# Optimization experiments

Measured on AMD Instinct MI355X. Metric: run time of the kernel, lower is better.

Reference implementation:

```python
import jax, jax.numpy as jnp
import numpy as np

PAD_VAL = -10000.0


def setup_inputs() -> dict:
    key = jax.random.key(0)
    k1, k2 = jax.random.split(key)
    B, C, H, W = 16, 3, 256, 256
    predicted = jax.random.normal(k1, (B, C, H, W), dtype=jnp.float32)
    ground_truth = jax.random.normal(k2, (B, C, H, W), dtype=jnp.float32)
    return {"predicted": predicted, "ground_truth": ground_truth, "nh": 5, "nw": 5}


def reference(predicted, ground_truth, nh, nw):
    # Faithful to torch: ConstantPad2d((v_pad, v_pad, h_pad, h_pad)) pads
    # W by v_pad = nh//2 and H by h_pad = nw//2 (symmetric when nh == nw).
    v_pad = nh // 2
    h_pad = nw // 2
    B, C, H, W = ground_truth.shape
    gt_pad = jnp.pad(
        ground_truth,
        ((0, 0), (0, 0), (h_pad, h_pad), (v_pad, v_pad)),
        constant_values=PAD_VAL,
    )
    # nh*nw shifted views of the padded ground truth: [B, C, H, W, nh*nw]
    refs = jnp.stack(
        [gt_pad[:, :, i:i + H, j:j + W] for i in range(nh) for j in range(nw)],
        axis=-1,
    )
    # L1 distance over channels for each neighbor shift: [B, H, W, nh*nw]
    norms = jnp.sum(jnp.abs(refs - predicted[..., None]), axis=1)
    # min over neighborhood, then mean over batch/spatial
    return jnp.mean(jnp.min(norms, axis=-1))
```

## Files before the change

kernel.cpp:

```cpp
#include <hip/hip_runtime.h>
#include <math.h>

#define PAD_VAL (-10000.0f)

constexpr int Cc = 3, Hh = 256, Ww = 256, Bb = 16;
constexpr int TW = 64;
constexpr int TH = 16;
constexpr int PXT = 4;
constexpr int LDSH = TH + 4;
constexpr int LDSW = 76;
constexpr int F4_PER_ROW = 18;
constexpr int NSLOT = Cc * LDSH * F4_PER_ROW;


__global__ __launch_bounds__(256) void nnloss_main(
    const float* __restrict__ pred, const float* __restrict__ gt,
    float* __restrict__ partial)
{
    __shared__ float sh[Cc][LDSH][LDSW];
    __shared__ float wsum[4];

    const int bx = blockIdx.x, by = blockIdx.y, b = blockIdx.z;
    const int cbase = bx * TW, rbase = by * TH;
    const int tid = threadIdx.x;
    const size_t base = (size_t)b * Cc * Hh * Ww;

    const bool interior = (bx >= 1) & (bx <= 2) & (by >= 1) & (by <= 14);
    if (interior) {
#pragma unroll
        for (int it = 0; it < 5; ++it) {
            int s = tid + it * 256;
            if (s < NSLOT) {
                int ch  = s / (LDSH * F4_PER_ROW);
                int rem = s - ch * (LDSH * F4_PER_ROW);
                int lr  = rem / F4_PER_ROW;
                int lc4 = rem - lr * F4_PER_ROW;
                int r   = rbase + lr - 2;
                int c   = cbase + lc4 * 4 - 4;
                float4 v = *reinterpret_cast<const float4*>(
                    &gt[base + ((size_t)ch * Hh + r) * Ww + c]);
                *reinterpret_cast<float4*>(&sh[ch][lr][lc4 * 4]) = v;
            }
        }
    } else {
#pragma unroll
        for (int it = 0; it < 5; ++it) {
            int s = tid + it * 256;
            if (s < NSLOT) {
                int ch  = s / (LDSH * F4_PER_ROW);
                int rem = s - ch * (LDSH * F4_PER_ROW);
                int lr  = rem / F4_PER_ROW;
                int lc4 = rem - lr * F4_PER_ROW;
                int r   = rbase + lr - 2;
                int c0  = cbase + lc4 * 4 - 4;
                float4 v;
                float* vp = reinterpret_cast<float*>(&v);
                const bool rok = (unsigned)r < (unsigned)Hh;
#pragma unroll
                for (int k = 0; k < 4; ++k) {
                    int c = c0 + k;
                    vp[k] = (rok && (unsigned)c < (unsigned)Ww)
                          ? gt[base + ((size_t)ch * Hh + r) * Ww + c] : PAD_VAL;
                }
                *reinterpret_cast<float4*>(&sh[ch][lr][lc4 * 4]) = v;
            }
        }
    }
    __syncthreads();

    const int gx  = tid & 15;
    const int gy  = tid >> 4;
    const int w0  = cbase + gx * PXT;
    const int row = rbase + gy;

    float p[Cc][PXT];
#pragma unroll
    for (int ch = 0; ch < Cc; ++ch) {
        float4 a = *reinterpret_cast<const float4*>(
            &pred[base + ((size_t)ch * Hh + row) * Ww + w0]);
        p[ch][0] = a.x; p[ch][1] = a.y; p[ch][2] = a.z; p[ch][3] = a.w;
    }

    float best[PXT];
#pragma unroll
    for (int px = 0; px < PXT; ++px) best[px] = 3.0e38f;

#pragma unroll
    for (int di = 0; di < 5; ++di) {
        float wv[Cc][12];
#pragma unroll
        for (int ch = 0; ch < Cc; ++ch) {
            const float4* q = reinterpret_cast<const float4*>(&sh[ch][gy + di][4 * gx]);
            float4 q0 = q[0], q1 = q[1], q2 = q[2];
            wv[ch][0] = q0.x; wv[ch][1]  = q0.y; wv[ch][2]  = q0.z; wv[ch][3]  = q0.w;
            wv[ch][4] = q1.x; wv[ch][5]  = q1.y; wv[ch][6]  = q1.z; wv[ch][7]  = q1.w;
            wv[ch][8] = q2.x; wv[ch][9]  = q2.y; wv[ch][10] = q2.z; wv[ch][11] = q2.w;
        }
#pragma unroll
        for (int dj = 0; dj < 5; ++dj) {
#pragma unroll
            for (int px = 0; px < PXT; ++px) {
                float s = fabsf(wv[0][px + dj + 2] - p[0][px])
                        + fabsf(wv[1][px + dj + 2] - p[1][px])
                        + fabsf(wv[2][px + dj + 2] - p[2][px]);
                best[px] = fminf(best[px], s);
            }
        }
    }

    float t = (best[0] + best[1]) + (best[2] + best[3]);
#pragma unroll
    for (int off = 32; off; off >>= 1) t += __shfl_down(t, off, 64);
    if ((tid & 63) == 0) wsum[tid >> 6] = t;
    __syncthreads();
    if (tid == 0) {
        int pid = (blockIdx.z * gridDim.y + blockIdx.y) * gridDim.x + blockIdx.x;
        partial[pid] = (wsum[0] + wsum[1]) + (wsum[2] + wsum[3]);
    }
}

__global__ __launch_bounds__(256) void nnloss_reduce(
    const float* __restrict__ partial, int n, float* __restrict__ out)
{
    __shared__ float ws[4];
    float t = 0.0f;
    for (int i = threadIdx.x; i < n; i += 256) t += partial[i];
#pragma unroll
    for (int off = 32; off; off >>= 1) t += __shfl_down(t, off, 64);
    if ((threadIdx.x & 63) == 0) ws[threadIdx.x >> 6] = t;
    __syncthreads();
    if (threadIdx.x == 0)
        out[0] = ((ws[0] + ws[1]) + (ws[2] + ws[3]))
               * (1.0f / ((float)Bb * (float)Hh * (float)Ww));
}

extern "C" void kernel_launch(void* const* d_in, const int* in_sizes, int n_in,
                              void* d_out, int out_size, void* d_ws, size_t ws_size,
                              hipStream_t stream) {
    const float* pred = (const float*)d_in[0];
    const float* gt   = (const float*)d_in[1];
    float* out     = (float*)d_out;
    float* partial = (float*)d_ws;

    dim3 grid(Ww / TW, Hh / TH, Bb);
    nnloss_main<<<grid, 256, 0, stream>>>(pred, gt, partial);
    nnloss_reduce<<<1, 256, 0, stream>>>(partial, 1024, out);
}
```

Measured before the change: 17.35 us.

## Compute two output rows per thread to reuse LDS window loads across rows

Halves the block to 128 threads, each handling a 2x4 pixel patch instead of 1x4, so each LDS window row is loaded once and reused by both output rows (6 row loads instead of 10). The separate interior and border gt-loading paths are merged into one float4 load guarded per vector, and the pred loads are issued before the LDS fill. This cuts LDS traffic and load count per pixel but raises register use and halves the threads per block, which may lower occupancy and latency hiding.

```diff
diff --git a/kernel.cpp b/kernel.cpp
--- a/kernel.cpp
+++ b/kernel.cpp
@@ -6,116 +6,104 @@
 constexpr int Cc = 3, Hh = 256, Ww = 256, Bb = 16;
 constexpr int TW = 64;
 constexpr int TH = 16;
-constexpr int PXT = 4;
 constexpr int LDSH = TH + 4;
 constexpr int LDSW = 76;
 constexpr int F4_PER_ROW = 18;
 constexpr int NSLOT = Cc * LDSH * F4_PER_ROW;
+constexpr int NTHR  = 128;
+constexpr int NBLK  = (Ww / TW) * (Hh / TH) * Bb;
 
 
-__global__ __launch_bounds__(256) void nnloss_main(
+__global__ __launch_bounds__(NTHR) void nnloss_main(
     const float* __restrict__ pred, const float* __restrict__ gt,
     float* __restrict__ partial)
 {
     __shared__ float sh[Cc][LDSH][LDSW];
-    __shared__ float wsum[4];
+    __shared__ float wsum[2];
 
     const int bx = blockIdx.x, by = blockIdx.y, b = blockIdx.z;
     const int cbase = bx * TW, rbase = by * TH;
     const int tid = threadIdx.x;
     const size_t base = (size_t)b * Cc * Hh * Ww;
 
-    const bool interior = (bx >= 1) & (bx <= 2) & (by >= 1) & (by <= 14);
-    if (interior) {
+    const int gx  = tid & 15;
+    const int ty  = tid >> 4;
+    const int pr0 = 2 * ty;
+    const int w0  = cbase + 4 * gx;
+    const int r0  = rbase + pr0;
+
+    float p[Cc][2][4];
 #pragma unroll
-        for (int it = 0; it < 5; ++it) {
-            int s = tid + it * 256;
-            if (s < NSLOT) {
-                int ch  = s / (LDSH * F4_PER_ROW);
-                int rem = s - ch * (LDSH * F4_PER_ROW);
-                int lr  = rem / F4_PER_ROW;
-                int lc4 = rem - lr * F4_PER_ROW;
-                int r   = rbase + lr - 2;
-                int c   = cbase + lc4 * 4 - 4;
-                float4 v = *reinterpret_cast<const float4*>(
-                    &gt[base + ((size_t)ch * Hh + r) * Ww + c]);
-                *reinterpret_cast<float4*>(&sh[ch][lr][lc4 * 4]) = v;
-            }
+    for (int ch = 0; ch < Cc; ++ch)
+#pragma unroll
+        for (int rr = 0; rr < 2; ++rr) {
+            float4 a = *reinterpret_cast<const float4*>(
+                &pred[base + ((size_t)ch * Hh + r0 + rr) * Ww + w0]);
+            p[ch][rr][0] = a.x; p[ch][rr][1] = a.y;
+            p[ch][rr][2] = a.z; p[ch][rr][3] = a.w;
         }
-    } else {
+
 #pragma unroll
-        for (int it = 0; it < 5; ++it) {
-            int s = tid + it * 256;
-            if (s < NSLOT) {
-                int ch  = s / (LDSH * F4_PER_ROW);
-                int rem = s - ch * (LDSH * F4_PER_ROW);
-                int lr  = rem / F4_PER_ROW;
-                int lc4 = rem - lr * F4_PER_ROW;
-                int r   = rbase + lr - 2;
-                int c0  = cbase + lc4 * 4 - 4;
-                float4 v;
-                float* vp = reinterpret_cast<float*>(&v);
-                const bool rok = (unsigned)r < (unsigned)Hh;
-#pragma unroll
-                for (int k = 0; k < 4; ++k) {
-                    int c = c0 + k;
-                    vp[k] = (rok && (unsigned)c < (unsigned)Ww)
-                          ? gt[base + ((size_t)ch * Hh + r) * Ww + c] : PAD_VAL;
-                }
-                *reinterpret_cast<float4*>(&sh[ch][lr][lc4 * 4]) = v;
-            }
+    for (int it = 0; it < 9; ++it) {
+        int s = tid + it * NTHR;
+        if (s < NSLOT) {
+            int ch  = s / (LDSH * F4_PER_ROW);
+            int rem = s - ch * (LDSH * F4_PER_ROW);
+            int lr  = rem / F4_PER_ROW;
+            int lc4 = rem - lr * F4_PER_ROW;
+            int r   = rbase + lr - 2;
+            int c0  = cbase + lc4 * 4 - 4;
+            float4 v = make_float4(PAD_VAL, PAD_VAL, PAD_VAL, PAD_VAL);
+            if (((unsigned)r < (unsigned)Hh) & ((unsigned)c0 < (unsigned)Ww))
+                v = *reinterpret_cast<const float4*>(
+                    &gt[base + ((size_t)ch * Hh + r) * Ww + c0]);
+            *reinterpret_cast<float4*>(&sh[ch][lr][lc4 * 4]) = v;
         }
     }
     __syncthreads();
 
-    const int gx  = tid & 15;
-    const int gy  = tid >> 4;
-    const int w0  = cbase + gx * PXT;
-    const int row = rbase + gy;
-
-    float p[Cc][PXT];
+    float best[2][4];
 #pragma unroll
-    for (int ch = 0; ch < Cc; ++ch) {
-        float4 a = *reinterpret_cast<const float4*>(
-            &pred[base + ((size_t)ch * Hh + row) * Ww + w0]);
-        p[ch][0] = a.x; p[ch][1] = a.y; p[ch][2] = a.z; p[ch][3] = a.w;
-    }
-
-    float best[PXT];
+    for (int rr = 0; rr < 2; ++rr)
 #pragma unroll
-    for (int px = 0; px < PXT; ++px) best[px] = 3.0e38f;
+        for (int px = 0; px < 4; ++px) best[rr][px] = 3.0e38f;
 
 #pragma unroll
-    for (int di = 0; di < 5; ++di) {
-        float wv[Cc][12];
+    for (int dr = 0; dr < 6; ++dr) {
+        float wr[Cc][12];
 #pragma unroll
         for (int ch = 0; ch < Cc; ++ch) {
-            const float4* q = reinterpret_cast<const float4*>(&sh[ch][gy + di][4 * gx]);
+            const float4* q = reinterpret_cast<const float4*>(&sh[ch][pr0 + dr][4 * gx]);
             float4 q0 = q[0], q1 = q[1], q2 = q[2];
-            wv[ch][0] = q0.x; wv[ch][1]  = q0.y; wv[ch][2]  = q0.z; wv[ch][3]  = q0.w;
-            wv[ch][4] = q1.x; wv[ch][5]  = q1.y; wv[ch][6]  = q1.z; wv[ch][7]  = q1.w;
-            wv[ch][8] = q2.x; wv[ch][9]  = q2.y; wv[ch][10] = q2.z; wv[ch][11] = q2.w;
+            wr[ch][0] = q0.x; wr[ch][1]  = q0.y; wr[ch][2]  = q0.z; wr[ch][3]  = q0.w;
+            wr[ch][4] = q1.x; wr[ch][5]  = q1.y; wr[ch][6]  = q1.z; wr[ch][7]  = q1.w;
+            wr[ch][8] = q2.x; wr[ch][9]  = q2.y; wr[ch][10] = q2.z; wr[ch][11] = q2.w;
         }
 #pragma unroll
-        for (int dj = 0; dj < 5; ++dj) {
+        for (int rr = 0; rr < 2; ++rr) {
+            if ((rr == 0 && dr <= 4) || (rr == 1 && dr >= 1)) {
 #pragma unroll
-            for (int px = 0; px < PXT; ++px) {
-                float s = fabsf(wv[0][px + dj + 2] - p[0][px])
-                        + fabsf(wv[1][px + dj + 2] - p[1][px])
-                        + fabsf(wv[2][px + dj + 2] - p[2][px]);
-                best[px] = fminf(best[px], s);
+                for (int dj = 0; dj < 5; ++dj)
+#pragma unroll
+                    for (int px = 0; px < 4; ++px) {
+                        float s = fabsf(wr[0][px + dj + 2] - p[0][rr][px])
+                                + fabsf(wr[1][px + dj + 2] - p[1][rr][px])
+                                + fabsf(wr[2][px + dj + 2] - p[2][rr][px]);
+                        best[rr][px] = fminf(best[rr][px], s);
+                    }
             }
         }
     }
 
-    float t = (best[0] + best[1]) + (best[2] + best[3]);
+    float t = ((best[0][0] + best[0][1]) + (best[0][2] + best[0][3]))
+            + ((best[1][0] + best[1][1]) + (best[1][2] + best[1][3]));
 #pragma unroll
     for (int off = 32; off; off >>= 1) t += __shfl_down(t, off, 64);
     if ((tid & 63) == 0) wsum[tid >> 6] = t;
     __syncthreads();
     if (tid == 0) {
         int pid = (blockIdx.z * gridDim.y + blockIdx.y) * gridDim.x + blockIdx.x;
-        partial[pid] = (wsum[0] + wsum[1]) + (wsum[2] + wsum[3]);
+        partial[pid] = wsum[0] + wsum[1];
     }
 }
 
@@ -143,6 +131,6 @@
     float* partial = (float*)d_ws;
 
     dim3 grid(Ww / TW, Hh / TH, Bb);
-    nnloss_main<<<grid, 256, 0, stream>>>(pred, gt, partial);
-    nnloss_reduce<<<1, 256, 0, stream>>>(partial, 1024, out);
+    nnloss_main<<<grid, NTHR, 0, stream>>>(pred, gt, partial);
+    nnloss_reduce<<<1, 256, 0, stream>>>(partial, NBLK, out);
 }
```

Result: faster. 16.90 us (-2.6%).
